# Optimization experiments

Measured on AMD Instinct MI355X. Metric: run time of the kernel, lower is better.

The kernel has to match this reference:

```python
import jax, jax.numpy as jnp
import numpy as np

B, T = 192, 50
VOCAB = 24000
EMBED = 300
HID2 = 2000          # 2*HIDDEN_SIZE
MAXOUT = 300         # DIMEN_MAXOUT_UNIT
QV = 300             # DIMEN_QUALITY_VECTOR
H2 = 100             # LSTM hidden


def setup_inputs():
    key = jax.random.key(0)
    ks = jax.random.split(key, 24)
    s = 0.02
    inp = {
        'dec_out': jax.random.normal(ks[0], (B, T, HID2), jnp.float32),
        'y': jax.random.randint(ks[1], (B, T), 0, VOCAB, jnp.int64 if jax.config.jax_enable_x64 else jnp.int32),
        'contex': jax.random.normal(ks[2], (B, T, HID2), jnp.float32),
        'embed_table': jax.random.normal(ks[3], (VOCAB, EMBED), jnp.float32) * s,
        'W1': jax.random.uniform(ks[4], (VOCAB, QV), jnp.float32),  # torch.rand
        'S_w': jax.random.normal(ks[5], (2 * MAXOUT, HID2), jnp.float32) * s,
        'S_b': jnp.zeros((2 * MAXOUT,), jnp.float32),
        'V_w': jax.random.normal(ks[6], (2 * MAXOUT, 2 * EMBED), jnp.float32) * s,
        'V_b': jnp.zeros((2 * MAXOUT,), jnp.float32),
        'C0_w': jax.random.normal(ks[7], (2 * MAXOUT, HID2), jnp.float32) * s,
        'C0_b': jnp.zeros((2 * MAXOUT,), jnp.float32),
        'W2_w': jax.random.normal(ks[8], (QV, MAXOUT), jnp.float32) * s,
        'W2_b': jnp.zeros((QV,), jnp.float32),
        'wih0': jax.random.normal(ks[9], (4 * H2, QV), jnp.float32) * s,
        'whh0': jax.random.normal(ks[10], (4 * H2, H2), jnp.float32) * s,
        'bih0': jnp.zeros((4 * H2,), jnp.float32),
        'bhh0': jnp.zeros((4 * H2,), jnp.float32),
        'wih1': jax.random.normal(ks[11], (4 * H2, H2), jnp.float32) * s,
        'whh1': jax.random.normal(ks[12], (4 * H2, H2), jnp.float32) * s,
        'bih1': jnp.zeros((4 * H2,), jnp.float32),
        'bhh1': jnp.zeros((4 * H2,), jnp.float32),
        'Wqe_w': jax.random.normal(ks[13], (1, H2), jnp.float32) * s,
        'Wqe_b': jnp.zeros((1,), jnp.float32),
    }
    return inp


def _lstm_layer(x, Wih, Whh, bih, bhh):
    # x: [B, T, D] -> outputs [B, T, H]; torch gate order i, f, g, o
    Bb = x.shape[0]
    H = Whh.shape[1]
    xT = jnp.swapaxes(x, 0, 1)  # [T, B, D]

    def step(carry, xt):
        h, c = carry
        g = xt @ Wih.T + h @ Whh.T + bih + bhh
        i, f, gg, o = jnp.split(g, 4, axis=-1)
        i = jax.nn.sigmoid(i); f = jax.nn.sigmoid(f)
        gg = jnp.tanh(gg); o = jax.nn.sigmoid(o)
        c = f * c + i * gg
        h = o * jnp.tanh(c)
        return (h, c), h

    h0 = jnp.zeros((Bb, H), x.dtype)
    (_, _), hs = jax.lax.scan(step, (h0, h0), xT)
    return jnp.swapaxes(hs, 0, 1)


def reference(dec_out, y, contex, embed_table, W1, S_w, S_b, V_w, V_b,
              C0_w, C0_b, W2_w, W2_b, wih0, whh0, bih0, bhh0,
              wih1, whh1, bih1, bhh1, Wqe_w, Wqe_b):
    Bb, Tt, _ = dec_out.shape
    embed = embed_table[y]  # [B, T, EMBED]
    idx = jnp.arange(Tt)
    li = jnp.where(idx == 0, 1, idx - 1)          # left neighbor (i==0 -> 1)
    ri = jnp.where(idx == Tt - 1, Tt - 2, idx + 1)  # right neighbor (i==T-1 -> T-2)
    tensor2 = jnp.concatenate([embed[:, li], embed[:, ri]], axis=-1)  # [B,T,600]
    t_long = (dec_out @ S_w.T + S_b) + (tensor2 @ V_w.T + V_b) + (contex @ C0_w.T + C0_b)
    # maxout over consecutive pairs: t[...,i] = max(t_long[...,2i], t_long[...,2i+1])
    t = t_long.reshape(Bb, Tt, MAXOUT, 2).max(axis=-1)
    a = t @ W2_w.T + W2_b                        # [B,T,QV]
    logits = a @ W1.T                            # [B,T,VOCAB]
    b = jax.nn.log_softmax(logits.reshape(Bb * Tt, -1), axis=1)
    quality = W1[y] * a                          # [B,T,QV]
    mask = (y == 0)
    index1 = jnp.where(mask.any(axis=1), mask.argmax(axis=1), Tt - 1)
    h = _lstm_layer(quality, wih0, whh0, bih0, bhh0)
    h = _lstm_layer(h, wih1, whh1, bih1, bhh1)   # [B,T,H2]
    s_sel = h[jnp.arange(Bb), index1]            # [B,H2]
    QE_score = jax.nn.sigmoid(s_sel @ Wqe_w.T + Wqe_b)  # [B,1]
    return (b, QE_score)
```

## Files before the change

kernel.cpp:

```cpp
#include <hip/hip_runtime.h>

typedef unsigned short u16;
typedef __attribute__((ext_vector_type(4))) float f32x4;
typedef __attribute__((ext_vector_type(8))) short bf16x8;
typedef __attribute__((ext_vector_type(4))) unsigned short u16x4;
typedef __attribute__((ext_vector_type(8))) unsigned short u16x8;

#define BT 9600
#define VOCAB 24000
#define NCB 188

__device__ __forceinline__ u16 f2b(float f){
  union { float f; unsigned u; } c; c.f = f;
  unsigned u = c.u;
  return (u16)((u + 0x7FFFu + ((u >> 16) & 1u)) >> 16);
}
__device__ __forceinline__ float b2f(u16 v){
  union { unsigned u; float f; } c; c.u = ((unsigned)v) << 16;
  return c.f;
}

#define GLD16(g, l) __builtin_amdgcn_global_load_lds( \
    (__attribute__((address_space(1))) void*)(g), \
    (__attribute__((address_space(3))) void*)(l), 16, 0, 0)

__device__ __forceinline__ void gemm_core(
    const u16* __restrict__ A, const u16* __restrict__ B,
    int K, int brow, int bcol, u16* As, u16* Bs, f32x4 acc[4][4])
{
  const int tid  = threadIdx.x;
  const int w    = tid >> 6;
  const int lane = tid & 63;
  const int wm = w >> 1, wn = w & 1;

  const f32x4 fz = {0.f, 0.f, 0.f, 0.f};
  #pragma unroll
  for (int m = 0; m < 4; ++m)
    #pragma unroll
    for (int n = 0; n < 4; ++n) acc[m][n] = fz;

  const int nkt = K >> 6;

  auto stage = [&](int kt, int buf) {
    #pragma unroll
    for (int i = 0; i < 4; ++i) {
      int gl  = i * 256 + tid;
      int row = gl >> 3;
      int g   = (gl & 7) ^ (row & 7);
      const u16* ga = A + (size_t)(brow + row) * K + (kt << 6) + (g << 3);
      GLD16(ga, As + buf * 8192 + (size_t)(i * 256 + w * 64) * 8);
      const u16* gb = B + (size_t)(bcol + row) * K + (kt << 6) + (g << 3);
      GLD16(gb, Bs + buf * 8192 + (size_t)(i * 256 + w * 64) * 8);
    }
  };

  stage(0, 0);
  int cur = 0;
  for (int kt = 0; kt < nkt; ++kt) {
    if (kt + 1 < nkt) {
      stage(kt + 1, cur ^ 1);
      asm volatile("s_waitcnt vmcnt(8)" ::: "memory");
    } else {
      asm volatile("s_waitcnt vmcnt(0)" ::: "memory");
    }
    __builtin_amdgcn_s_barrier();
    asm volatile("" ::: "memory");
    const u16* Ab = As + cur * 8192;
    const u16* Bb = Bs + cur * 8192;
    #pragma unroll
    for (int kk = 0; kk < 2; ++kk) {
      bf16x8 af[4], bf[4];
      #pragma unroll
      for (int m = 0; m < 4; ++m) {
        int row = wm * 64 + m * 16 + (lane & 15);
        int g   = (kk * 4 + (lane >> 4)) ^ (row & 7);
        af[m] = *(const bf16x8*)(Ab + row * 64 + g * 8);
      }
      #pragma unroll
      for (int n = 0; n < 4; ++n) {
        int row = wn * 64 + n * 16 + (lane & 15);
        int g   = (kk * 4 + (lane >> 4)) ^ (row & 7);
        bf[n] = *(const bf16x8*)(Bb + row * 64 + g * 8);
      }
      #pragma unroll
      for (int m = 0; m < 4; ++m)
        #pragma unroll
        for (int n = 0; n < 4; ++n)
          acc[m][n] = __builtin_amdgcn_mfma_f32_16x16x32_bf16(af[m], bf[n], acc[m][n], 0, 0, 0);
    }
    asm volatile("" ::: "memory");
    __builtin_amdgcn_s_barrier();
    cur ^= 1;
  }
}

__device__ __forceinline__ void prep_main_body(
    const float* __restrict__ dec, const float* __restrict__ ctx,
    u16* __restrict__ Xcat, int tid)
{
  if (tid >= 9600 * 500) return;
  int r = tid / 500, k8 = (tid % 500) * 8;
  const float* src = (k8 < 2000) ? dec + (size_t)r * 2000 + k8
                                 : ctx + (size_t)r * 2000 + (k8 - 2000);
  const float4* s4 = (const float4*)src;
  float4 v0 = s4[0], v1 = s4[1];
  u16x8 o;
  o[0] = f2b(v0.x); o[1] = f2b(v0.y); o[2] = f2b(v0.z); o[3] = f2b(v0.w);
  o[4] = f2b(v1.x); o[5] = f2b(v1.y); o[6] = f2b(v1.z); o[7] = f2b(v1.w);
  *(u16x8*)(Xcat + (size_t)r * 4608 + k8) = o;
}

__device__ __forceinline__ void prep_emb_body(
    const int* __restrict__ y, const float* __restrict__ etab,
    u16* __restrict__ Xcat, int tid)
{
  if (tid >= 9600 * 152) return;
  int r = tid / 152, u = tid % 152;
  u16* xr = Xcat + (size_t)r * 4608;
  if (u >= 150) {
    int base = (u == 150) ? 4300 : 4604;
    u16x4 z; z[0] = 0; z[1] = 0; z[2] = 0; z[3] = 0;
    *(u16x4*)(xr + base) = z;
    return;
  }
  int t = r % 50;
  int side = u / 75, j4 = (u % 75) * 4;
  int tt = (side == 0) ? (t == 0 ? 1 : t - 1) : (t == 49 ? 48 : t + 1);
  int tok = y[r - t + tt];
  float4 v = *(const float4*)(etab + (size_t)tok * 300 + j4);
  u16x4 o; o[0] = f2b(v.x); o[1] = f2b(v.y); o[2] = f2b(v.z); o[3] = f2b(v.w);
  *(u16x4*)(xr + (side == 0 ? 4000 : 4304) + j4) = o;
}

__device__ __forceinline__ void wcat_body(
    const float* __restrict__ Sw, const float* __restrict__ C0w, const float* __restrict__ Vw,
    const float* __restrict__ Sb, const float* __restrict__ Vb, const float* __restrict__ C0b,
    u16* __restrict__ Wcat, float* __restrict__ biasc, int tid)
{
  if (tid >= 640 * 4608) return;
  int n = tid / 4608, k = tid % 4608;
  float v = 0.f;
  if (n < 600) {
    if (k < 2000)                  v = Sw[n * 2000 + k];
    else if (k < 4000)             v = C0w[n * 2000 + (k - 2000)];
    else if (k < 4300)             v = Vw[n * 600 + (k - 4000)];
    else if (k >= 4304 && k < 4604) v = Vw[n * 600 + 300 + (k - 4304)];
  }
  Wcat[tid] = f2b(v);
  if (k == 0) biasc[n] = (n < 600) ? (Sb[n] + Vb[n] + C0b[n]) : 0.f;
}

__device__ __forceinline__ void conv_body(
    const float* __restrict__ src, u16* __restrict__ dst,
    int srows, int scols, int drows, int dcols4, int tid)
{
  if (tid >= drows * dcols4) return;
  int r = tid / dcols4, c4 = (tid % dcols4) * 4;
  u16x4 o; o[0] = 0; o[1] = 0; o[2] = 0; o[3] = 0;
  if (r < srows && c4 < scols) {
    float4 v = *(const float4*)(src + (size_t)r * scols + c4);
    o[0] = f2b(v.x); o[1] = f2b(v.y); o[2] = f2b(v.z); o[3] = f2b(v.w);
  }
  *(u16x4*)(dst + (size_t)r * (dcols4 * 4) + c4) = o;
}

__global__ __launch_bounds__(256) void k_prep_all(
    const float* __restrict__ dec, const float* __restrict__ ctx,
    const int* __restrict__ y, const float* __restrict__ etab,
    const float* __restrict__ Sw, const float* __restrict__ C0w,
    const float* __restrict__ Vw, const float* __restrict__ Sb,
    const float* __restrict__ Vb, const float* __restrict__ C0b,
    const float* __restrict__ W1, const float* __restrict__ W2w,
    const float* __restrict__ wih0, const float* __restrict__ wih1,
    u16* __restrict__ Xcat, u16* __restrict__ Wcat, float* __restrict__ biasc,
    u16* __restrict__ W1b, u16* __restrict__ W2b,
    u16* __restrict__ wih0b, u16* __restrict__ wih1b)
{
  int bid = blockIdx.x, th = threadIdx.x;
  if (bid < 18750)      prep_main_body(dec, ctx, Xcat, bid * 256 + th);
  else if (bid < 24450) prep_emb_body(y, etab, Xcat, (bid - 18750) * 256 + th);
  else if (bid < 35970) wcat_body(Sw, C0w, Vw, Sb, Vb, C0b, Wcat, biasc, (bid - 24450) * 256 + th);
  else if (bid < 43490) conv_body(W1,   W1b,   24000, 300, 24064, 80, (bid - 35970) * 256 + th);
  else if (bid < 43610) conv_body(W2w,  W2b,   300,   300, 384,   80, (bid - 43490) * 256 + th);
  else if (bid < 43770) conv_body(wih0, wih0b, 400,   300, 512,   80, (bid - 43610) * 256 + th);
  else                  conv_body(wih1, wih1b, 400,   100, 512,   32, (bid - 43770) * 256 + th);
}

__global__ __launch_bounds__(256) void k_gemm_tlong(
    const u16* __restrict__ Xcat, const u16* __restrict__ Wcat,
    const float* __restrict__ biasc, u16* __restrict__ tb)
{
  __shared__ u16 As[16384], Bs[16384];
  f32x4 acc[4][4];
  int brow = blockIdx.y * 128, bcol = blockIdx.x * 128;
  gemm_core(Xcat, Wcat, 4608, brow, bcol, As, Bs, acc);
  int lane = threadIdx.x & 63, w = threadIdx.x >> 6;
  int wm = w >> 1, wn = w & 1;
  #pragma unroll
  for (int m = 0; m < 4; ++m)
    #pragma unroll
    for (int n = 0; n < 4; ++n)
      #pragma unroll
      for (int r = 0; r < 4; ++r) {
        int row = brow + wm * 64 + m * 16 + ((lane >> 4) << 2) + r;
        int col = bcol + wn * 64 + n * 16 + (lane & 15);
        float v = acc[m][n][r] + biasc[col];
        float o = __shfl_xor(v, 1);
        float t = fmaxf(v, o);
        if ((lane & 1) == 0)
          tb[(size_t)row * 320 + (col >> 1)] = f2b(t);
      }
}

__global__ __launch_bounds__(256) void k_gemm_a(
    const u16* __restrict__ tb, const u16* __restrict__ W2b,
    const float* __restrict__ W2bias, const float* __restrict__ W1,
    const int* __restrict__ y, u16* __restrict__ ab, u16* __restrict__ qb)
{
  __shared__ u16 As[16384], Bs[16384];
  f32x4 acc[4][4];
  int brow = blockIdx.y * 128, bcol = blockIdx.x * 128;
  gemm_core(tb, W2b, 320, brow, bcol, As, Bs, acc);
  int lane = threadIdx.x & 63, w = threadIdx.x >> 6;
  int wm = w >> 1, wn = w & 1;
  #pragma unroll
  for (int m = 0; m < 4; ++m)
    #pragma unroll
    for (int n = 0; n < 4; ++n)
      #pragma unroll
      for (int r = 0; r < 4; ++r) {
        int row = brow + wm * 64 + m * 16 + ((lane >> 4) << 2) + r;
        int col = bcol + wn * 64 + n * 16 + (lane & 15);
        if (col < 320) {
          float bias = (col < 300) ? W2bias[col] : 0.f;
          float a = acc[m][n][r] + bias;
          ab[(size_t)row * 320 + col] = f2b(a);
          float q = 0.f;
          if (col < 300) {
            int yv = y[row];
            q = a * W1[(size_t)yv * 300 + col];
          }
          qb[(size_t)row * 320 + col] = f2b(q);
        }
      }
}

__global__ __launch_bounds__(256) void k_gemm_logits_bf16(
    const u16* __restrict__ ab, const u16* __restrict__ W1b,
    u16* __restrict__ lb, float* __restrict__ part, int rb0)
{
  __shared__ u16 smem[32768];
  __shared__ float rowsum[128][2];
  f32x4 acc[4][4];
  int brow = (rb0 + blockIdx.y) * 128, bcol = blockIdx.x * 128;
  gemm_core(ab, W1b, 320, brow, bcol, smem, smem + 16384, acc);
  int lane = threadIdx.x & 63, w = threadIdx.x >> 6;
  int wm = w >> 1, wn = w & 1;
  #pragma unroll
  for (int m = 0; m < 4; ++m)
    #pragma unroll
    for (int r = 0; r < 4; ++r) {
      int lrow = wm * 64 + m * 16 + ((lane >> 4) << 2) + r;
      float es = 0.f;
      #pragma unroll
      for (int n = 0; n < 4; ++n) {
        int lcol = wn * 64 + n * 16 + (lane & 15);
        float v = acc[m][n][r];
        smem[lrow * 136 + lcol] = f2b(v);
        if (bcol + lcol < VOCAB) es += __expf(v);
      }
      es += __shfl_xor(es, 1); es += __shfl_xor(es, 2);
      es += __shfl_xor(es, 4); es += __shfl_xor(es, 8);
      if ((lane & 15) == 0) rowsum[lrow][wn] = es;
    }
  __syncthreads();
  if (threadIdx.x < 128)
    part[(size_t)(brow + threadIdx.x) * NCB + blockIdx.x] =
        rowsum[threadIdx.x][0] + rowsum[threadIdx.x][1];
  int lrow_base = blockIdx.y * 128;
  #pragma unroll
  for (int j = 0; j < 8; ++j) {
    int ch   = j * 256 + threadIdx.x;
    int rowl = ch >> 4;
    int c16  = (ch & 15) << 3;
    u16x8 v = *(const u16x8*)(smem + rowl * 136 + c16);
    *(u16x8*)(lb + (size_t)(lrow_base + rowl) * 24064 + bcol + c16) = v;
  }
}

__global__ __launch_bounds__(256) void k_gemm_logits_f32(
    const u16* __restrict__ ab, const u16* __restrict__ W1b,
    float* __restrict__ dout, float* __restrict__ part)
{
  __shared__ u16 As[16384], Bs[16384];
  __shared__ float rowsum[128][2];
  f32x4 acc[4][4];
  int brow = blockIdx.y * 128, bcol = blockIdx.x * 128;
  gemm_core(ab, W1b, 320, brow, bcol, As, Bs, acc);
  int lane = threadIdx.x & 63, w = threadIdx.x >> 6;
  int wm = w >> 1, wn = w & 1;
  #pragma unroll
  for (int m = 0; m < 4; ++m)
    #pragma unroll
    for (int r = 0; r < 4; ++r) {
      int lrow = wm * 64 + m * 16 + ((lane >> 4) << 2) + r;
      size_t grow = (size_t)(brow + lrow);
      float es = 0.f;
      #pragma unroll
      for (int n = 0; n < 4; ++n) {
        int col = bcol + wn * 64 + n * 16 + (lane & 15);
        float v = acc[m][n][r];
        if (col < VOCAB) {
          dout[grow * VOCAB + col] = v;
          es += __expf(v);
        }
      }
      es += __shfl_xor(es, 1); es += __shfl_xor(es, 2);
      es += __shfl_xor(es, 4); es += __shfl_xor(es, 8);
      if ((lane & 15) == 0) rowsum[lrow][wn] = es;
    }
  __syncthreads();
  if (threadIdx.x < 128)
    part[(size_t)(brow + threadIdx.x) * NCB + blockIdx.x] =
        rowsum[threadIdx.x][0] + rowsum[threadIdx.x][1];
}

__global__ __launch_bounds__(256) void k_gemm_proj(
    const u16* __restrict__ Ab, const u16* __restrict__ Bb, int K,
    const float* __restrict__ b1, const float* __restrict__ b2, float* __restrict__ out)
{
  __shared__ u16 As[16384], Bs[16384];
  f32x4 acc[4][4];
  int brow = blockIdx.y * 128, bcol = blockIdx.x * 128;
  gemm_core(Ab, Bb, K, brow, bcol, As, Bs, acc);
  int lane = threadIdx.x & 63, w = threadIdx.x >> 6;
  int wm = w >> 1, wn = w & 1;
  #pragma unroll
  for (int m = 0; m < 4; ++m)
    #pragma unroll
    for (int n = 0; n < 4; ++n)
      #pragma unroll
      for (int r = 0; r < 4; ++r) {
        int row = brow + wm * 64 + m * 16 + ((lane >> 4) << 2) + r;
        int col = bcol + wn * 64 + n * 16 + (lane & 15);
        if (col < 400)
          out[(size_t)row * 400 + col] = acc[m][n][r] + b1[col] + b2[col];
      }
}

__global__ __launch_bounds__(256) void k_rowlog(
    const float* __restrict__ part, float* __restrict__ logl, int r0)
{
  int row = r0 + blockIdx.x * 4 + (threadIdx.x >> 6);
  int l = threadIdx.x & 63;
  const float* p = part + (size_t)row * NCB;
  float s = p[l] + p[l + 64] + (l < 60 ? p[l + 128] : 0.f);
  s += __shfl_xor(s, 1);  s += __shfl_xor(s, 2);  s += __shfl_xor(s, 4);
  s += __shfl_xor(s, 8);  s += __shfl_xor(s, 16); s += __shfl_xor(s, 32);
  if (l == 0) logl[row] = logf(s);
}

__global__ __launch_bounds__(256) void k_fixup(
    float4* __restrict__ out4, const float* __restrict__ logl)
{
  size_t i = (size_t)blockIdx.x * blockDim.x + threadIdx.x;
  size_t stride = (size_t)gridDim.x * blockDim.x;
  const size_t total = (size_t)BT * (VOCAB / 4);
  for (; i < total; i += stride) {
    size_t row = i / (VOCAB / 4);
    float l = logl[row];
    float4 v = out4[i];
    v.x -= l; v.y -= l; v.z -= l; v.w -= l;
    out4[i] = v;
  }
}

__global__ __launch_bounds__(256) void k_fixup_bf16(
    const u16* __restrict__ lb, const float* __restrict__ logl,
    float* __restrict__ out, int r0, int nrows)
{
  size_t i = (size_t)blockIdx.x * blockDim.x + threadIdx.x;
  size_t stride = (size_t)gridDim.x * blockDim.x;
  const size_t total = (size_t)nrows * (VOCAB / 8);
  for (; i < total; i += stride) {
    size_t rowl = i / (VOCAB / 8);
    int c8 = (int)(i % (VOCAB / 8)) * 8;
    size_t row = r0 + rowl;
    float l = logl[row];
    u16x8 v = *(const u16x8*)(lb + rowl * 24064 + c8);
    float4 o0, o1;
    o0.x = b2f(v[0]) - l; o0.y = b2f(v[1]) - l; o0.z = b2f(v[2]) - l; o0.w = b2f(v[3]) - l;
    o1.x = b2f(v[4]) - l; o1.y = b2f(v[5]) - l; o1.z = b2f(v[6]) - l; o1.w = b2f(v[7]) - l;
    float* op = out + row * VOCAB + c8;
    *(float4*)op = o0;
    *(float4*)(op + 4) = o1;
  }
}

__global__ __launch_bounds__(512) void k_lstm0(
    const float* __restrict__ xp0, const float* __restrict__ whh0, u16* __restrict__ h0b)
{
  int b = blockIdx.x, g = threadIdx.x;
  __shared__ float h[100];
  __shared__ float act[400];
  float wrow[100];
  if (g < 400) {
    const float4* wr = (const float4*)(whh0 + (size_t)g * 100);
    #pragma unroll
    for (int q = 0; q < 25; ++q) {
      float4 t = wr[q];
      wrow[4 * q] = t.x; wrow[4 * q + 1] = t.y; wrow[4 * q + 2] = t.z; wrow[4 * q + 3] = t.w;
    }
  }
  if (g < 100) h[g] = 0.f;
  float c = 0.f;
  __syncthreads();
  for (int t = 0; t < 50; ++t) {
    if (g < 400) {
      float s = xp0[(size_t)(b * 50 + t) * 400 + g];
      const float4* hv = (const float4*)h;
      #pragma unroll
      for (int q = 0; q < 25; ++q) {
        float4 hh = hv[q];
        s += wrow[4 * q] * hh.x + wrow[4 * q + 1] * hh.y
           + wrow[4 * q + 2] * hh.z + wrow[4 * q + 3] * hh.w;
      }
      act[g] = (g >= 200 && g < 300) ? tanhf(s) : 1.f / (1.f + __expf(-s));
    }
    __syncthreads();
    if (g < 100) {
      c = act[100 + g] * c + act[g] * act[200 + g];
      float hn = act[300 + g] * tanhf(c);
      h[g] = hn;
      h0b[(size_t)(b * 50 + t) * 128 + g] = f2b(hn);
    } else if (g < 128) {
      h0b[(size_t)(b * 50 + t) * 128 + g] = 0;
    }
    __syncthreads();
  }
}

__global__ __launch_bounds__(512) void k_lstm1(
    const float* __restrict__ xp1, const float* __restrict__ whh1,
    const int* __restrict__ y, const float* __restrict__ wqe,
    const float* __restrict__ wqeb, float* __restrict__ qout)
{
  int b = blockIdx.x, g = threadIdx.x;
  __shared__ float h[100];
  __shared__ float act[400];
  __shared__ float hsel[100];
  __shared__ int idx1;
  float wrow[100];
  if (g < 400) {
    const float4* wr = (const float4*)(whh1 + (size_t)g * 100);
    #pragma unroll
    for (int q = 0; q < 25; ++q) {
      float4 t = wr[q];
      wrow[4 * q] = t.x; wrow[4 * q + 1] = t.y; wrow[4 * q + 2] = t.z; wrow[4 * q + 3] = t.w;
    }
  }
  if (g == 0) {
    int ix = 49;
    for (int t = 0; t < 50; ++t) { if (y[b * 50 + t] == 0) { ix = t; break; } }
    idx1 = ix;
  }
  if (g < 100) { h[g] = 0.f; hsel[g] = 0.f; }
  float c = 0.f;
  __syncthreads();
  for (int t = 0; t < 50; ++t) {
    if (g < 400) {
      float s = xp1[(size_t)(b * 50 + t) * 400 + g];
      const float4* hv = (const float4*)h;
      #pragma unroll
      for (int q = 0; q < 25; ++q) {
        float4 hh = hv[q];
        s += wrow[4 * q] * hh.x + wrow[4 * q + 1] * hh.y
           + wrow[4 * q + 2] * hh.z + wrow[4 * q + 3] * hh.w;
      }
      act[g] = (g >= 200 && g < 300) ? tanhf(s) : 1.f / (1.f + __expf(-s));
    }
    __syncthreads();
    if (g < 100) {
      c = act[100 + g] * c + act[g] * act[200 + g];
      float hn = act[300 + g] * tanhf(c);
      h[g] = hn;
      if (t == idx1) hsel[g] = hn;
    }
    __syncthreads();
  }
  if (g == 0) {
    float s = wqeb[0];
    for (int j = 0; j < 100; ++j) s += hsel[j] * wqe[j];
    qout[b] = 1.f / (1.f + __expf(-s));
  }
}

extern "C" void kernel_launch(void* const* d_in, const int* in_sizes, int n_in,
                              void* d_out, int out_size, void* d_ws, size_t ws_size,
                              hipStream_t stream) {
  const float* dec  = (const float*)d_in[0];
  const int*   y    = (const int*)d_in[1];
  const float* ctx  = (const float*)d_in[2];
  const float* etab = (const float*)d_in[3];
  const float* W1   = (const float*)d_in[4];
  const float* Sw   = (const float*)d_in[5];
  const float* Sb   = (const float*)d_in[6];
  const float* Vw   = (const float*)d_in[7];
  const float* Vb   = (const float*)d_in[8];
  const float* C0w  = (const float*)d_in[9];
  const float* C0b  = (const float*)d_in[10];
  const float* W2w  = (const float*)d_in[11];
  const float* W2bias = (const float*)d_in[12];
  const float* wih0 = (const float*)d_in[13];
  const float* whh0 = (const float*)d_in[14];
  const float* bih0 = (const float*)d_in[15];
  const float* bhh0 = (const float*)d_in[16];
  const float* wih1 = (const float*)d_in[17];
  const float* whh1 = (const float*)d_in[18];
  const float* bih1 = (const float*)d_in[19];
  const float* bhh1 = (const float*)d_in[20];
  const float* wqe  = (const float*)d_in[21];
  const float* wqeb = (const float*)d_in[22];

  char* ws = (char*)d_ws;
  u16*   Xcat  = (u16*)(ws + 0);
  u16*   Wcat  = (u16*)(ws + 88473600);
  float* biasc = (float*)(ws + 94371840);
  u16*   tb    = (u16*)(ws + 94374400);
  u16*   W2b   = (u16*)(ws + 100518400);
  u16*   ab    = (u16*)(ws + 100764160);
  u16*   qb    = (u16*)(ws + 106908160);
  u16*   W1b   = (u16*)(ws + 113052160);
  float* part  = (float*)(ws + 128453120);
  float* logl  = (float*)(ws + 135672320);
  u16*   wih0b = (u16*)(ws + 135710720);
  float* xp0   = (float*)(ws + 136038400);
  u16*   h0b   = (u16*)(ws + 151398400);
  u16*   wih1b = (u16*)(ws + 153856000);
  float* xp1   = (float*)(ws + 153987072);
  u16*   lb    = (u16*)(ws + 169347072);
  const size_t WS_NEED_BF16 = 169347072ull + 154009600ull;
  const bool use_bf16_logits = (ws_size >= WS_NEED_BF16);

  float* bout  = (float*)d_out;
  float* qeout = bout + (size_t)BT * VOCAB;

  k_prep_all<<<43834, 256, 0, stream>>>(dec, ctx, y, etab, Sw, C0w, Vw, Sb, Vb, C0b,
                                        W1, W2w, wih0, wih1,
                                        Xcat, Wcat, biasc, W1b, W2b, wih0b, wih1b);

  k_gemm_tlong<<<dim3(5, 75), 256, 0, stream>>>(Xcat, Wcat, biasc, tb);
  k_gemm_a<<<dim3(3, 75), 256, 0, stream>>>(tb, W2b, W2bias, W1, y, ab, qb);

  if (use_bf16_logits) {
    for (int c = 0; c < 3; ++c) {
      k_gemm_logits_bf16<<<dim3(NCB, 25), 256, 0, stream>>>(ab, W1b, lb, part, 25 * c);
      k_rowlog<<<800, 256, 0, stream>>>(part, logl, 3200 * c);
      k_fixup_bf16<<<2048, 256, 0, stream>>>(lb, logl, bout, 3200 * c, 3200);
    }
  } else {
    k_gemm_logits_f32<<<dim3(NCB, 75), 256, 0, stream>>>(ab, W1b, bout, part);
    k_rowlog<<<2400, 256, 0, stream>>>(part, logl, 0);
    k_fixup<<<4096, 256, 0, stream>>>((float4*)bout, logl);
  }

  k_gemm_proj<<<dim3(4, 75), 256, 0, stream>>>(qb, wih0b, 320, bih0, bhh0, xp0);
  k_lstm0<<<192, 512, 0, stream>>>(xp0, whh0, h0b);
  k_gemm_proj<<<dim3(4, 75), 256, 0, stream>>>(h0b, wih1b, 128, bih1, bhh1, xp1);
  k_lstm1<<<192, 512, 0, stream>>>(xp1, whh1, y, wqe, wqeb, qeout);
}
```

Measured before the change: 1.048 ms.

## Unchunk bf16 logits pipeline and remap tlong GEMM blocks across XCDs

The bf16 logits path drops its three-chunk loop. It now runs one GEMM over all 9600 rows with a flat 1D grid, then one row-logsum pass and one fixup pass, using a full-size bf16 logits buffer. This cuts launch count and serialization between chunks. In exchange it needs a much larger workspace, and the intermediate no longer stays cache-resident between the GEMM and the fixup. The t_long GEMM also gets a 1D grid that groups row tiles by XCD (id & 7) for L2 locality, which leaves a few blocks idle.

```diff
diff --git a/kernel.cpp b/kernel.cpp
--- a/kernel.cpp
+++ b/kernel.cpp
@@ -28,7 +28,7 @@
     const u16* __restrict__ A, const u16* __restrict__ B,
     int K, int brow, int bcol, u16* As, u16* Bs, f32x4 acc[4][4])
 {
-  const int tid  = threadIdx.x;
+  const int tid  = threadIdx.x & 255;
   const int w    = tid >> 6;
   const int lane = tid & 63;
   const int wm = w >> 1, wn = w & 1;
@@ -48,9 +48,9 @@
       int row = gl >> 3;
       int g   = (gl & 7) ^ (row & 7);
       const u16* ga = A + (size_t)(brow + row) * K + (kt << 6) + (g << 3);
-      GLD16(ga, As + buf * 8192 + (size_t)(i * 256 + w * 64) * 8);
+      GLD16(ga, As + buf * 8192 + gl * 8);
       const u16* gb = B + (size_t)(bcol + row) * K + (kt << 6) + (g << 3);
-      GLD16(gb, Bs + buf * 8192 + (size_t)(i * 256 + w * 64) * 8);
+      GLD16(gb, Bs + buf * 8192 + gl * 8);
     }
   };
 
@@ -92,6 +92,27 @@
     __builtin_amdgcn_s_barrier();
     cur ^= 1;
   }
+}
+
+__device__ __forceinline__ void proj_epilogue(
+    f32x4 acc[4][4], int brow, int bcol,
+    const float* __restrict__ b1, const float* __restrict__ b2,
+    float* __restrict__ out)
+{
+  int tid = threadIdx.x & 255;
+  int lane = tid & 63, w = tid >> 6;
+  int wm = w >> 1, wn = w & 1;
+  #pragma unroll
+  for (int m = 0; m < 4; ++m)
+    #pragma unroll
+    for (int n = 0; n < 4; ++n)
+      #pragma unroll
+      for (int r = 0; r < 4; ++r) {
+        int row = brow + wm * 64 + m * 16 + ((lane >> 4) << 2) + r;
+        int col = bcol + wn * 64 + n * 16 + (lane & 15);
+        if (col < 400)
+          out[(size_t)row * 400 + col] = acc[m][n][r] + b1[col] + b2[col];
+      }
 }
 
 __device__ __forceinline__ void prep_main_body(
@@ -192,7 +213,12 @@
 {
   __shared__ u16 As[16384], Bs[16384];
   f32x4 acc[4][4];
-  int brow = blockIdx.y * 128, bcol = blockIdx.x * 128;
+  int L = blockIdx.x;
+  int xcd = L & 7, s = L >> 3;
+  int yy = (s / 5) * 8 + xcd;
+  int xx = s % 5;
+  if (yy >= 75) return;
+  int brow = yy * 128, bcol = xx * 128;
   gemm_core(Xcat, Wcat, 4608, brow, bcol, As, Bs, acc);
   int lane = threadIdx.x & 63, w = threadIdx.x >> 6;
   int wm = w >> 1, wn = w & 1;
@@ -245,14 +271,15 @@
       }
 }
 
-__global__ __launch_bounds__(256) void k_gemm_logits_bf16(
+__global__ __launch_bounds__(256) void k_gemm_logits(
     const u16* __restrict__ ab, const u16* __restrict__ W1b,
-    u16* __restrict__ lb, float* __restrict__ part, int rb0)
+    u16* __restrict__ lb, float* __restrict__ part)
 {
   __shared__ u16 smem[32768];
   __shared__ float rowsum[128][2];
   f32x4 acc[4][4];
-  int brow = (rb0 + blockIdx.y) * 128, bcol = blockIdx.x * 128;
+  int g = blockIdx.x;
+  int brow = (g / NCB) * 128, bcol = (g % NCB) * 128;
   gemm_core(ab, W1b, 320, brow, bcol, smem, smem + 16384, acc);
   int lane = threadIdx.x & 63, w = threadIdx.x >> 6;
   int wm = w >> 1, wn = w & 1;
@@ -275,16 +302,157 @@
     }
   __syncthreads();
   if (threadIdx.x < 128)
-    part[(size_t)(brow + threadIdx.x) * NCB + blockIdx.x] =
+    part[(size_t)(brow + threadIdx.x) * NCB + (g % NCB)] =
         rowsum[threadIdx.x][0] + rowsum[threadIdx.x][1];
-  int lrow_base = blockIdx.y * 128;
   #pragma unroll
   for (int j = 0; j < 8; ++j) {
     int ch   = j * 256 + threadIdx.x;
     int rowl = ch >> 4;
     int c16  = (ch & 15) << 3;
     u16x8 v = *(const u16x8*)(smem + rowl * 136 + c16);
-    *(u16x8*)(lb + (size_t)(lrow_base + rowl) * 24064 + bcol + c16) = v;
+    *(u16x8*)(lb + (size_t)(brow + rowl) * 24064 + bcol + c16) = v;
+  }
+}
+
+__global__ __launch_bounds__(256) void k_rowlog(
+    const float* __restrict__ part, float* __restrict__ logl)
+{
+  int row = blockIdx.x * 4 + (threadIdx.x >> 6);
+  int l = threadIdx.x & 63;
+  const float* p = part + (size_t)row * NCB;
+  float s = p[l] + p[l + 64] + (l < 60 ? p[l + 128] : 0.f);
+  s += __shfl_xor(s, 1);  s += __shfl_xor(s, 2);  s += __shfl_xor(s, 4);
+  s += __shfl_xor(s, 8);  s += __shfl_xor(s, 16); s += __shfl_xor(s, 32);
+  if (l == 0) logl[row] = logf(s);
+}
+
+__global__ __launch_bounds__(256) void k_fixup_bf16(
+    const u16* __restrict__ lb, const float* __restrict__ logl,
+    float* __restrict__ out)
+{
+  size_t i = (size_t)blockIdx.x * blockDim.x + threadIdx.x;
+  size_t stride = (size_t)gridDim.x * blockDim.x;
+  const size_t total = (size_t)BT * (VOCAB / 8);
+  for (; i < total; i += stride) {
+    size_t row = i / (VOCAB / 8);
+    int c8 = (int)(i % (VOCAB / 8)) * 8;
+    float l = logl[row];
+    u16x8 v = *(const u16x8*)(lb + row * 24064 + c8);
+    float4 o0, o1;
+    o0.x = b2f(v[0]) - l; o0.y = b2f(v[1]) - l; o0.z = b2f(v[2]) - l; o0.w = b2f(v[3]) - l;
+    o1.x = b2f(v[4]) - l; o1.y = b2f(v[5]) - l; o1.z = b2f(v[6]) - l; o1.w = b2f(v[7]) - l;
+    float* op = out + row * VOCAB + c8;
+    *(float4*)op = o0;
+    *(float4*)(op + 4) = o1;
+  }
+}
+
+__global__ __launch_bounds__(256) void k_gemm_proj(
+    const u16* __restrict__ Ab, const u16* __restrict__ Bb, int K,
+    const float* __restrict__ b1, const float* __restrict__ b2, float* __restrict__ out)
+{
+  __shared__ u16 As[16384], Bs[16384];
+  f32x4 acc[4][4];
+  int brow = blockIdx.y * 128, bcol = blockIdx.x * 128;
+  gemm_core(Ab, Bb, K, brow, bcol, As, Bs, acc);
+  proj_epilogue(acc, brow, bcol, b1, b2, out);
+}
+
+__global__ __launch_bounds__(512) void k_lstm0(
+    const float* __restrict__ xp0, const float* __restrict__ whh0, u16* __restrict__ h0b)
+{
+  int b = blockIdx.x, g = threadIdx.x;
+  __shared__ float h[100];
+  __shared__ float act[400];
+  float wrow[100];
+  if (g < 400) {
+    const float4* wr = (const float4*)(whh0 + (size_t)g * 100);
+    #pragma unroll
+    for (int q = 0; q < 25; ++q) {
+      float4 t = wr[q];
+      wrow[4 * q] = t.x; wrow[4 * q + 1] = t.y; wrow[4 * q + 2] = t.z; wrow[4 * q + 3] = t.w;
+    }
+  }
+  if (g < 100) h[g] = 0.f;
+  float c = 0.f;
+  __syncthreads();
+  for (int t = 0; t < 50; ++t) {
+    if (g < 400) {
+      float s = xp0[(size_t)(b * 50 + t) * 400 + g];
+      const float4* hv = (const float4*)h;
+      #pragma unroll
+      for (int q = 0; q < 25; ++q) {
+        float4 hh = hv[q];
+        s += wrow[4 * q] * hh.x + wrow[4 * q + 1] * hh.y
+           + wrow[4 * q + 2] * hh.z + wrow[4 * q + 3] * hh.w;
+      }
+      act[g] = (g >= 200 && g < 300) ? tanhf(s) : 1.f / (1.f + __expf(-s));
+    }
+    __syncthreads();
+    if (g < 100) {
+      c = act[100 + g] * c + act[g] * act[200 + g];
+      float hn = act[300 + g] * tanhf(c);
+      h[g] = hn;
+      h0b[(size_t)(b * 50 + t) * 128 + g] = f2b(hn);
+    } else if (g < 128) {
+      h0b[(size_t)(b * 50 + t) * 128 + g] = 0;
+    }
+    __syncthreads();
+  }
+}
+
+__global__ __launch_bounds__(512) void k_lstm1(
+    const float* __restrict__ xp1, const float* __restrict__ whh1,
+    const int* __restrict__ y, const float* __restrict__ wqe,
+    const float* __restrict__ wqeb, float* __restrict__ qout)
+{
+  int b = blockIdx.x, g = threadIdx.x;
+  __shared__ float h[100];
+  __shared__ float act[400];
+  __shared__ float hsel[100];
+  __shared__ int idx1;
+  float wrow[100];
+  if (g < 400) {
+    const float4* wr = (const float4*)(whh1 + (size_t)g * 100);
+    #pragma unroll
+    for (int q = 0; q < 25; ++q) {
+      float4 t = wr[q];
+      wrow[4 * q] = t.x; wrow[4 * q + 1] = t.y; wrow[4 * q + 2] = t.z; wrow[4 * q + 3] = t.w;
+    }
+  }
+  if (g == 0) {
+    int ix = 49;
+    for (int t = 0; t < 50; ++t) { if (y[b * 50 + t] == 0) { ix = t; break; } }
+    idx1 = ix;
+  }
+  if (g < 100) { h[g] = 0.f; hsel[g] = 0.f; }
+  float c = 0.f;
+  __syncthreads();
+  for (int t = 0; t < 50; ++t) {
+    if (g < 400) {
+      float s = xp1[(size_t)(b * 50 + t) * 400 + g];
+      const float4* hv = (const float4*)h;
+      #pragma unroll
+      for (int q = 0; q < 25; ++q) {
+        float4 hh = hv[q];
+        s += wrow[4 * q] * hh.x + wrow[4 * q + 1] * hh.y
+           + wrow[4 * q + 2] * hh.z + wrow[4 * q + 3] * hh.w;
+      }
+      act[g] = (g >= 200 && g < 300) ? tanhf(s) : 1.f / (1.f + __expf(-s));
+    }
+    __syncthreads();
+    if (g < 100) {
+      c = act[100 + g] * c + act[g] * act[200 + g];
+      float hn = act[300 + g] * tanhf(c);
+      h[g] = hn;
+      if (t == idx1) hsel[g] = hn;
+    }
+    __syncthreads();
+  }
+  if (g == 0) {
+    float s = wqeb[0];
+    for (int j = 0; j < 100; ++j) s += hsel[j] * wqe[j];
+    qout[b] = 1.f / (1.f + __expf(-s));
   }
 }
 
@@ -310,10 +478,7 @@
       for (int n = 0; n < 4; ++n) {
         int col = bcol + wn * 64 + n * 16 + (lane & 15);
         float v = acc[m][n][r];
-        if (col < VOCAB) {
-          dout[grow * VOCAB + col] = v;
-          es += __expf(v);
-        }
+        if (col < VOCAB) { dout[grow * VOCAB + col] = v; es += __expf(v); }
       }
       es += __shfl_xor(es, 1); es += __shfl_xor(es, 2);
       es += __shfl_xor(es, 4); es += __shfl_xor(es, 8);
@@ -325,42 +490,7 @@
         rowsum[threadIdx.x][0] + rowsum[threadIdx.x][1];
 }
 
-__global__ __launch_bounds__(256) void k_gemm_proj(
-    const u16* __restrict__ Ab, const u16* __restrict__ Bb, int K,
-    const float* __restrict__ b1, const float* __restrict__ b2, float* __restrict__ out)
-{
-  __shared__ u16 As[16384], Bs[16384];
-  f32x4 acc[4][4];
-  int brow = blockIdx.y * 128, bcol = blockIdx.x * 128;
-  gemm_core(Ab, Bb, K, brow, bcol, As, Bs, acc);
-  int lane = threadIdx.x & 63, w = threadIdx.x >> 6;
-  int wm = w >> 1, wn = w & 1;
-  #pragma unroll
-  for (int m = 0; m < 4; ++m)
-    #pragma unroll
-    for (int n = 0; n < 4; ++n)
-      #pragma unroll
-      for (int r = 0; r < 4; ++r) {
-        int row = brow + wm * 64 + m * 16 + ((lane >> 4) << 2) + r;
-        int col = bcol + wn * 64 + n * 16 + (lane & 15);
-        if (col < 400)
-          out[(size_t)row * 400 + col] = acc[m][n][r] + b1[col] + b2[col];
-      }
-}
-
-__global__ __launch_bounds__(256) void k_rowlog(
-    const float* __restrict__ part, float* __restrict__ logl, int r0)
-{
-  int row = r0 + blockIdx.x * 4 + (threadIdx.x >> 6);
-  int l = threadIdx.x & 63;
-  const float* p = part + (size_t)row * NCB;
-  float s = p[l] + p[l + 64] + (l < 60 ? p[l + 128] : 0.f);
-  s += __shfl_xor(s, 1);  s += __shfl_xor(s, 2);  s += __shfl_xor(s, 4);
-  s += __shfl_xor(s, 8);  s += __shfl_xor(s, 16); s += __shfl_xor(s, 32);
-  if (l == 0) logl[row] = logf(s);
-}
-
-__global__ __launch_bounds__(256) void k_fixup(
+__global__ __launch_bounds__(256) void k_fixup_f32(
     float4* __restrict__ out4, const float* __restrict__ logl)
 {
   size_t i = (size_t)blockIdx.x * blockDim.x + threadIdx.x;
@@ -372,126 +502,6 @@
     float4 v = out4[i];
     v.x -= l; v.y -= l; v.z -= l; v.w -= l;
     out4[i] = v;
-  }
-}
-
-__global__ __launch_bounds__(256) void k_fixup_bf16(
-    const u16* __restrict__ lb, const float* __restrict__ logl,
-    float* __restrict__ out, int r0, int nrows)
-{
-  size_t i = (size_t)blockIdx.x * blockDim.x + threadIdx.x;
-  size_t stride = (size_t)gridDim.x * blockDim.x;
-  const size_t total = (size_t)nrows * (VOCAB / 8);
-  for (; i < total; i += stride) {
-    size_t rowl = i / (VOCAB / 8);
-    int c8 = (int)(i % (VOCAB / 8)) * 8;
-    size_t row = r0 + rowl;
-    float l = logl[row];
-    u16x8 v = *(const u16x8*)(lb + rowl * 24064 + c8);
-    float4 o0, o1;
-    o0.x = b2f(v[0]) - l; o0.y = b2f(v[1]) - l; o0.z = b2f(v[2]) - l; o0.w = b2f(v[3]) - l;
-    o1.x = b2f(v[4]) - l; o1.y = b2f(v[5]) - l; o1.z = b2f(v[6]) - l; o1.w = b2f(v[7]) - l;
-    float* op = out + row * VOCAB + c8;
-    *(float4*)op = o0;
-    *(float4*)(op + 4) = o1;
-  }
-}
-
-__global__ __launch_bounds__(512) void k_lstm0(
-    const float* __restrict__ xp0, const float* __restrict__ whh0, u16* __restrict__ h0b)
-{
-  int b = blockIdx.x, g = threadIdx.x;
-  __shared__ float h[100];
-  __shared__ float act[400];
-  float wrow[100];
-  if (g < 400) {
-    const float4* wr = (const float4*)(whh0 + (size_t)g * 100);
-    #pragma unroll
-    for (int q = 0; q < 25; ++q) {
-      float4 t = wr[q];
-      wrow[4 * q] = t.x; wrow[4 * q + 1] = t.y; wrow[4 * q + 2] = t.z; wrow[4 * q + 3] = t.w;
-    }
-  }
-  if (g < 100) h[g] = 0.f;
-  float c = 0.f;
-  __syncthreads();
-  for (int t = 0; t < 50; ++t) {
-    if (g < 400) {
-      float s = xp0[(size_t)(b * 50 + t) * 400 + g];
-      const float4* hv = (const float4*)h;
-      #pragma unroll
-      for (int q = 0; q < 25; ++q) {
-        float4 hh = hv[q];
-        s += wrow[4 * q] * hh.x + wrow[4 * q + 1] * hh.y
-           + wrow[4 * q + 2] * hh.z + wrow[4 * q + 3] * hh.w;
-      }
-      act[g] = (g >= 200 && g < 300) ? tanhf(s) : 1.f / (1.f + __expf(-s));
-    }
-    __syncthreads();
-    if (g < 100) {
-      c = act[100 + g] * c + act[g] * act[200 + g];
-      float hn = act[300 + g] * tanhf(c);
-      h[g] = hn;
-      h0b[(size_t)(b * 50 + t) * 128 + g] = f2b(hn);
-    } else if (g < 128) {
-      h0b[(size_t)(b * 50 + t) * 128 + g] = 0;
-    }
-    __syncthreads();
-  }
-}
-
-__global__ __launch_bounds__(512) void k_lstm1(
-    const float* __restrict__ xp1, const float* __restrict__ whh1,
-    const int* __restrict__ y, const float* __restrict__ wqe,
-    const float* __restrict__ wqeb, float* __restrict__ qout)
-{
-  int b = blockIdx.x, g = threadIdx.x;
-  __shared__ float h[100];
-  __shared__ float act[400];
-  __shared__ float hsel[100];
-  __shared__ int idx1;
-  float wrow[100];
-  if (g < 400) {
-    const float4* wr = (const float4*)(whh1 + (size_t)g * 100);
-    #pragma unroll
-    for (int q = 0; q < 25; ++q) {
-      float4 t = wr[q];
-      wrow[4 * q] = t.x; wrow[4 * q + 1] = t.y; wrow[4 * q + 2] = t.z; wrow[4 * q + 3] = t.w;
-    }
-  }
-  if (g == 0) {
-    int ix = 49;
-    for (int t = 0; t < 50; ++t) { if (y[b * 50 + t] == 0) { ix = t; break; } }
-    idx1 = ix;
-  }
-  if (g < 100) { h[g] = 0.f; hsel[g] = 0.f; }
-  float c = 0.f;
-  __syncthreads();
-  for (int t = 0; t < 50; ++t) {
-    if (g < 400) {
-      float s = xp1[(size_t)(b * 50 + t) * 400 + g];
-      const float4* hv = (const float4*)h;
-      #pragma unroll
-      for (int q = 0; q < 25; ++q) {
-        float4 hh = hv[q];
-        s += wrow[4 * q] * hh.x + wrow[4 * q + 1] * hh.y
-           + wrow[4 * q + 2] * hh.z + wrow[4 * q + 3] * hh.w;
-      }
-      act[g] = (g >= 200 && g < 300) ? tanhf(s) : 1.f / (1.f + __expf(-s));
-    }
-    __syncthreads();
-    if (g < 100) {
-      c = act[100 + g] * c + act[g] * act[200 + g];
-      float hn = act[300 + g] * tanhf(c);
-      h[g] = hn;
-      if (t == idx1) hsel[g] = hn;
-    }
-    __syncthreads();
-  }
-  if (g == 0) {
-    float s = wqeb[0];
-    for (int j = 0; j < 100; ++j) s += hsel[j] * wqe[j];
-    qout[b] = 1.f / (1.f + __expf(-s));
   }
 }
 
@@ -539,7 +549,7 @@
   u16*   wih1b = (u16*)(ws + 153856000);
   float* xp1   = (float*)(ws + 153987072);
   u16*   lb    = (u16*)(ws + 169347072);
-  const size_t WS_NEED_BF16 = 169347072ull + 154009600ull;
+  const size_t WS_NEED_BF16 = 169347072ull + 462028800ull;
   const bool use_bf16_logits = (ws_size >= WS_NEED_BF16);
 
   float* bout  = (float*)d_out;
@@ -549,19 +559,18 @@
                                         W1, W2w, wih0, wih1,
                                         Xcat, Wcat, biasc, W1b, W2b, wih0b, wih1b);
 
-  k_gemm_tlong<<<dim3(5, 75), 256, 0, stream>>>(Xcat, Wcat, biasc, tb);
+  k_gemm_tlong<<<400, 256, 0, stream>>>(Xcat, Wcat, biasc, tb);
   k_gemm_a<<<dim3(3, 75), 256, 0, stream>>>(tb, W2b, W2bias, W1, y, ab, qb);
 
   if (use_bf16_logits) {
-    for (int c = 0; c < 3; ++c) {
-      k_gemm_logits_bf16<<<dim3(NCB, 25), 256, 0, stream>>>(ab, W1b, lb, part, 25 * c);
-      k_rowlog<<<800, 256, 0, stream>>>(part, logl, 3200 * c);
-      k_fixup_bf16<<<2048, 256, 0, stream>>>(lb, logl, bout, 3200 * c, 3200);
-    }
+    k_gemm_logits<<<14100, 256, 0, stream>>>(ab, W1b, lb, part);
+    k_rowlog<<<2400, 256, 0, stream>>>(part, logl);
+    k_fixup_bf16<<<4096, 256, 0, stream>>>(lb, logl, bout);
   } else {
-    k_gemm_logits_f32<<<dim3(NCB, 75), 256, 0, stream>>>(ab, W1b, bout, part);
-    k_rowlog<<<2400, 256, 0, stream>>>(part, logl, 0);
-    k_fixup<<<4096, 256, 0, stream>>>((float4*)bout, logl);
+    float* part_fb = (float*)(ws + 169347072);
+    k_gemm_logits_f32<<<dim3(NCB, 75), 256, 0, stream>>>(ab, W1b, bout, part_fb);
+    k_rowlog<<<2400, 256, 0, stream>>>(part_fb, logl);
+    k_fixup_f32<<<4096, 256, 0, stream>>>((float4*)bout, logl);
   }
 
   k_gemm_proj<<<dim3(4, 75), 256, 0, stream>>>(qb, wih0b, 320, bih0, bhh0, xp0);
```

Measured after the change: 986.6 us. 5.9% less time.
